# Kernel optimization log

Measured on AMD Instinct MI355X. Metric: run time of the kernel, lower is better.

Reference implementation:

```python
import jax, jax.numpy as jnp
import numpy as np

B, T, N, H, DK = 4, 16, 256, 8, 64

def setup_inputs() -> dict:
    key = jax.random.key(0)
    k1, k2, k3 = jax.random.split(key, 3)
    queries = jax.random.normal(k1, (B, T, N, H, DK), dtype=jnp.float32)
    keys = jax.random.normal(k2, (B, T, N, H, DK), dtype=jnp.float32)
    values = jax.random.normal(k3, (B, T, N, H, DK), dtype=jnp.float32)
    attention_mask = jnp.zeros((B, T, 1, N, N), dtype=bool)  # unused: mask_flag=False
    return {"queries": queries, "keys": keys, "values": values, "attention_mask": attention_mask}

def reference(queries, keys, values, attention_mask):
    # queries: B T N H d_k; keys/values: B T S H d_k/d_v
    d_k = queries.shape[-1]
    scale = 1.0 / jnp.sqrt(jnp.asarray(d_k, queries.dtype))
    # scores: B T H N S
    scores = jnp.einsum('btnhe,btshe->bthns', queries, keys)
    # mask_flag=False -> no masking; dropout is identity in eval mode
    A = jax.nn.softmax(scale * scores, axis=-1)
    V = jnp.einsum('bthns,btshd->btnhd', A, values)
    return V
```

## Files before the change

### kernel.cpp

```cpp
#include <hip/hip_runtime.h>


typedef short short8 __attribute__((ext_vector_type(8)));
typedef float floatx16 __attribute__((ext_vector_type(16)));

__device__ __forceinline__ unsigned cvt_pk(float lo, float hi) {
  unsigned r;
  asm("v_cvt_pk_bf16_f32 %0, %1, %2" : "=v"(r) : "v"(lo), "v"(hi));
  return r;
}

constexpr int KSTR  = 72;
constexpr int VSTRW = 132;

__global__ __launch_bounds__(512, 2) void attn_kernel(
    const float* __restrict__ Q, const float* __restrict__ K,
    const float* __restrict__ V, float* __restrict__ O) {
  __shared__ __align__(16) short    Klds[256 * KSTR];
  __shared__ __align__(16) unsigned Vt32[64 * VSTRW];

  const int inst = blockIdx.x;
  const int h8   = inst & 7;
  const int bt   = inst >> 3;
  const int base = bt * (256 * 512) + h8 * 64;
  const int tid  = threadIdx.x;

  const int wave = tid >> 6;
  const int lane = tid & 63;
  const int r31  = lane & 31;
  const int h    = lane >> 5;
  const int c4   = tid & 15;
  const int sQ   = tid >> 4;

  {
    const float* Kb = K + base;
    #pragma unroll
    for (int i = 0; i < 8; ++i) {
      int idx = i * 512 + tid;
      int s = idx >> 4, cc = idx & 15;
      float4 v = *reinterpret_cast<const float4*>(Kb + s * 512 + cc * 4);
      uint2 w;
      w.x = cvt_pk(v.x, v.y);
      w.y = cvt_pk(v.z, v.w);
      *reinterpret_cast<uint2*>(&Klds[s * KSTR + cc * 4]) = w;
    }
  }
  {
    const float* Vb = V + base;
    #pragma unroll
    for (int i = 0; i < 4; ++i) {
      int idx = i * 512 + tid;
      int sp = idx >> 4, cc = idx & 15;
      int s = sp * 2;
      int spw = sp ^ ((cc & 7) << 2);
      float4 v0 = *reinterpret_cast<const float4*>(Vb + s * 512 + cc * 4);
      float4 v1 = *reinterpret_cast<const float4*>(Vb + (s + 1) * 512 + cc * 4);
      #pragma unroll
      for (int k = 0; k < 4; ++k)
        Vt32[(cc * 4 + k) * VSTRW + spw] = cvt_pk((&v0.x)[k], (&v1.x)[k]);
    }
  }

  const float SCQ = 0.125f * 1.4426950408889634f;
  const int nq = wave * 32 + r31;
  short8 qf[4];
  #pragma unroll
  for (int kc = 0; kc < 4; ++kc) {
    const float* qp = Q + base + nq * 512 + 16 * kc + 8 * h;
    float4 a = *reinterpret_cast<const float4*>(qp);
    float4 b = *reinterpret_cast<const float4*>(qp + 4);
    union { unsigned u[4]; short8 s; } t;
    t.u[0] = cvt_pk(a.x * SCQ, a.y * SCQ);
    t.u[1] = cvt_pk(a.z * SCQ, a.w * SCQ);
    t.u[2] = cvt_pk(b.x * SCQ, b.y * SCQ);
    t.u[3] = cvt_pk(b.z * SCQ, b.w * SCQ);
    qf[kc] = t.s;
  }
  __syncthreads();

  const int swzr = ((r31 >> 2) & 7) << 2;

  floatx16 ao0 = {}, ao1 = {};
  float ps[4] = {0.f, 0.f, 0.f, 0.f};

  #pragma unroll
  for (int it = 0; it < 8; ++it) {
    floatx16 sc = {};
    #pragma unroll
    for (int kc = 0; kc < 4; ++kc) {
      short8 kf = *reinterpret_cast<const short8*>(
          &Klds[(32 * it + r31) * KSTR + 16 * kc + 8 * h]);
      sc = __builtin_amdgcn_mfma_f32_32x32x16_bf16(kf, qf[kc], sc, 0, 0, 0);
    }

    unsigned pk[8];
    #pragma unroll
    for (int q = 0; q < 4; ++q) {
      float e0 = exp2f(sc[4 * q + 0]);
      float e1 = exp2f(sc[4 * q + 1]);
      float e2 = exp2f(sc[4 * q + 2]);
      float e3 = exp2f(sc[4 * q + 3]);
      ps[q] += (e0 + e1) + (e2 + e3);
      pk[2 * q]     = cvt_pk(e0, e1);
      pk[2 * q + 1] = cvt_pk(e2, e3);
    }

    union { unsigned u[4]; short8 s; } pa0, pa1;
    {
      unsigned x, y;
      x = pk[0]; y = pk[2];
      asm("v_permlane32_swap_b32 %0, %1" : "+v"(x), "+v"(y));
      pa0.u[0] = x; pa0.u[2] = y;
      x = pk[1]; y = pk[3];
      asm("v_permlane32_swap_b32 %0, %1" : "+v"(x), "+v"(y));
      pa0.u[1] = x; pa0.u[3] = y;
      x = pk[4]; y = pk[6];
      asm("v_permlane32_swap_b32 %0, %1" : "+v"(x), "+v"(y));
      pa1.u[0] = x; pa1.u[2] = y;
      x = pk[5]; y = pk[7];
      asm("v_permlane32_swap_b32 %0, %1" : "+v"(x), "+v"(y));
      pa1.u[1] = x; pa1.u[3] = y;
    }

    {
      const unsigned* vrow0 = &Vt32[(r31) * VSTRW];
      const unsigned* vrow1 = &Vt32[(32 + r31) * VSTRW];
      short8 vf00 = *reinterpret_cast<const short8*>(
          vrow0 + ((16 * it + 4 * h) ^ swzr));
      short8 vf01 = *reinterpret_cast<const short8*>(
          vrow0 + ((16 * it + 8 + 4 * h) ^ swzr));
      short8 vf10 = *reinterpret_cast<const short8*>(
          vrow1 + ((16 * it + 4 * h) ^ swzr));
      short8 vf11 = *reinterpret_cast<const short8*>(
          vrow1 + ((16 * it + 8 + 4 * h) ^ swzr));
      ao0 = __builtin_amdgcn_mfma_f32_32x32x16_bf16(pa0.s, vf00, ao0, 0, 0, 0);
      ao0 = __builtin_amdgcn_mfma_f32_32x32x16_bf16(pa1.s, vf01, ao0, 0, 0, 0);
      ao1 = __builtin_amdgcn_mfma_f32_32x32x16_bf16(pa0.s, vf10, ao1, 0, 0, 0);
      ao1 = __builtin_amdgcn_mfma_f32_32x32x16_bf16(pa1.s, vf11, ao1, 0, 0, 0);
    }
  }

  float pstot = (ps[0] + ps[1]) + (ps[2] + ps[3]);
  pstot += __shfl_xor(pstot, 32);
  const float rcp = __builtin_amdgcn_rcpf(pstot);

  float rcpv[16];
  #pragma unroll
  for (int reg = 0; reg < 16; ++reg)
    rcpv[reg] = __shfl(rcp, (reg & 3) + 8 * (reg >> 2) + 4 * h);

  #pragma unroll
  for (int reg = 0; reg < 16; ++reg) {
    int n = wave * 32 + (reg & 3) + 8 * (reg >> 2) + 4 * h;
    O[base + n * 512 + r31]      = ao0[reg] * rcpv[reg];
    O[base + n * 512 + 32 + r31] = ao1[reg] * rcpv[reg];
  }
}

extern "C" void kernel_launch(void* const* d_in, const int* in_sizes, int n_in,
                              void* d_out, int out_size, void* d_ws, size_t ws_size,
                              hipStream_t stream) {
  const float* Q = (const float*)d_in[0];
  const float* K = (const float*)d_in[1];
  const float* V = (const float*)d_in[2];
  float* O = (float*)d_out;
  attn_kernel<<<dim3(512), dim3(512), 0, stream>>>(Q, K, V, O);
}
```

Before: 33.80 us.

## Process two heads per block with double-buffered LDS and 16x16 MFMA tiles

Each 1024-thread block now handles two (bt,head) instances. K/V for the second instance are staged into a second LDS buffer while the first is being computed, which is meant to hide global load latency. The attention math switches from 32x32x16 to 16x16x32 MFMAs with 16 queries per wave, using permlane16/32 swaps to rebuild the P operand. The grid is halved to 256 blocks, which cuts the number of active workgroups on a 256-CU part and raises register and LDS pressure per block.

```diff
diff --git a/kernel.cpp b/kernel.cpp
--- a/kernel.cpp
+++ b/kernel.cpp
@@ -2,7 +2,7 @@
 
 
 typedef short short8 __attribute__((ext_vector_type(8)));
-typedef float floatx16 __attribute__((ext_vector_type(16)));
+typedef float floatx4 __attribute__((ext_vector_type(4)));
 
 __device__ __forceinline__ unsigned cvt_pk(float lo, float hi) {
   unsigned r;
@@ -13,148 +13,151 @@
 constexpr int KSTR  = 72;
 constexpr int VSTRW = 132;
 
-__global__ __launch_bounds__(512, 2) void attn_kernel(
+__device__ __forceinline__ void stage_kv(const float* __restrict__ Kb,
+                                         const float* __restrict__ Vb,
+                                         short* Kl, unsigned* Vt, int tid) {
+  #pragma unroll
+  for (int i = 0; i < 4; ++i) {
+    int idx = i * 1024 + tid;
+    int s = idx >> 4, cc = idx & 15;
+    float4 v = *reinterpret_cast<const float4*>(Kb + s * 512 + cc * 4);
+    uint2 w;
+    w.x = cvt_pk(v.x, v.y);
+    w.y = cvt_pk(v.z, v.w);
+    *reinterpret_cast<uint2*>(&Kl[s * KSTR + cc * 4]) = w;
+  }
+  #pragma unroll
+  for (int i = 0; i < 2; ++i) {
+    int idx = i * 1024 + tid;
+    int sp = idx >> 4, cc = idx & 15;
+    int s = sp * 2;
+    int spw = sp ^ ((cc & 7) << 2);
+    float4 v0 = *reinterpret_cast<const float4*>(Vb + s * 512 + cc * 4);
+    float4 v1 = *reinterpret_cast<const float4*>(Vb + (s + 1) * 512 + cc * 4);
+    #pragma unroll
+    for (int k = 0; k < 4; ++k)
+      Vt[(cc * 4 + k) * VSTRW + spw] = cvt_pk((&v0.x)[k], (&v1.x)[k]);
+  }
+}
+
+__global__ __launch_bounds__(1024, 4) void attn_kernel(
     const float* __restrict__ Q, const float* __restrict__ K,
     const float* __restrict__ V, float* __restrict__ O) {
-  __shared__ __align__(16) short    Klds[256 * KSTR];
-  __shared__ __align__(16) unsigned Vt32[64 * VSTRW];
+  __shared__ __align__(16) short    Klds[2][256 * KSTR];
+  __shared__ __align__(16) unsigned Vt32[2][64 * VSTRW];
 
-  const int inst = blockIdx.x;
-  const int h8   = inst & 7;
-  const int bt   = inst >> 3;
-  const int base = bt * (256 * 512) + h8 * 64;
   const int tid  = threadIdx.x;
-
   const int wave = tid >> 6;
   const int lane = tid & 63;
-  const int r31  = lane & 31;
-  const int h    = lane >> 5;
-  const int c4   = tid & 15;
-  const int sQ   = tid >> 4;
+  const int c    = lane & 15;
+  const int g    = lane >> 4;
 
-  {
-    const float* Kb = K + base;
-    #pragma unroll
-    for (int i = 0; i < 8; ++i) {
-      int idx = i * 512 + tid;
-      int s = idx >> 4, cc = idx & 15;
-      float4 v = *reinterpret_cast<const float4*>(Kb + s * 512 + cc * 4);
-      uint2 w;
-      w.x = cvt_pk(v.x, v.y);
-      w.y = cvt_pk(v.z, v.w);
-      *reinterpret_cast<uint2*>(&Klds[s * KSTR + cc * 4]) = w;
-    }
-  }
-  {
-    const float* Vb = V + base;
-    #pragma unroll
-    for (int i = 0; i < 4; ++i) {
-      int idx = i * 512 + tid;
-      int sp = idx >> 4, cc = idx & 15;
-      int s = sp * 2;
-      int spw = sp ^ ((cc & 7) << 2);
-      float4 v0 = *reinterpret_cast<const float4*>(Vb + s * 512 + cc * 4);
-      float4 v1 = *reinterpret_cast<const float4*>(Vb + (s + 1) * 512 + cc * 4);
-      #pragma unroll
-      for (int k = 0; k < 4; ++k)
-        Vt32[(cc * 4 + k) * VSTRW + spw] = cvt_pk((&v0.x)[k], (&v1.x)[k]);
-    }
+  const int i0    = blockIdx.x * 2;
+  const int i1    = i0 + 1;
+  const int base0 = (i0 >> 3) * (256 * 512) + (i0 & 7) * 64;
+  const int base1 = (i1 >> 3) * (256 * 512) + (i1 & 7) * 64;
+
+  const float SCQ = 0.125f * 1.4426950408889634f;
+
+#define LOADQ(qf, gbase)                                                     \
+  {                                                                          \
+    _Pragma("unroll")                                                        \
+    for (int ks2 = 0; ks2 < 2; ++ks2) {                                      \
+      const float* qp = Q + (gbase) + (wave * 16 + c) * 512 + ks2 * 32 + g * 8; \
+      float4 a  = *reinterpret_cast<const float4*>(qp);                      \
+      float4 bb = *reinterpret_cast<const float4*>(qp + 4);                  \
+      union { unsigned u[4]; short8 s; } t;                                  \
+      t.u[0] = cvt_pk(a.x * SCQ, a.y * SCQ);                                 \
+      t.u[1] = cvt_pk(a.z * SCQ, a.w * SCQ);                                 \
+      t.u[2] = cvt_pk(bb.x * SCQ, bb.y * SCQ);                               \
+      t.u[3] = cvt_pk(bb.z * SCQ, bb.w * SCQ);                               \
+      qf[ks2] = t.s;                                                         \
+    }                                                                        \
   }
 
-  const float SCQ = 0.125f * 1.4426950408889634f;
-  const int nq = wave * 32 + r31;
-  short8 qf[4];
-  #pragma unroll
-  for (int kc = 0; kc < 4; ++kc) {
-    const float* qp = Q + base + nq * 512 + 16 * kc + 8 * h;
-    float4 a = *reinterpret_cast<const float4*>(qp);
-    float4 b = *reinterpret_cast<const float4*>(qp + 4);
-    union { unsigned u[4]; short8 s; } t;
-    t.u[0] = cvt_pk(a.x * SCQ, a.y * SCQ);
-    t.u[1] = cvt_pk(a.z * SCQ, a.w * SCQ);
-    t.u[2] = cvt_pk(b.x * SCQ, b.y * SCQ);
-    t.u[3] = cvt_pk(b.z * SCQ, b.w * SCQ);
-    qf[kc] = t.s;
+#define COMPUTE(b, qf, ao, ps)                                               \
+  _Pragma("unroll")                                                          \
+  for (int ks = 0; ks < 8; ++ks) {                                           \
+    unsigned pk2[2][2];                                                      \
+    _Pragma("unroll")                                                        \
+    for (int tt = 0; tt < 2; ++tt) {                                         \
+      const int t = 2 * ks + tt;                                             \
+      short8 kf0 = *reinterpret_cast<const short8*>(                         \
+          &Klds[b][(t * 16 + c) * KSTR + g * 8]);                            \
+      short8 kf1 = *reinterpret_cast<const short8*>(                         \
+          &Klds[b][(t * 16 + c) * KSTR + 32 + g * 8]);                       \
+      floatx4 acc = {0.f, 0.f, 0.f, 0.f};                                    \
+      acc = __builtin_amdgcn_mfma_f32_16x16x32_bf16(kf0, qf[0], acc, 0, 0, 0); \
+      acc = __builtin_amdgcn_mfma_f32_16x16x32_bf16(kf1, qf[1], acc, 0, 0, 0); \
+      float e0 = exp2f(acc[0]);                                              \
+      float e1 = exp2f(acc[1]);                                              \
+      float e2 = exp2f(acc[2]);                                              \
+      float e3 = exp2f(acc[3]);                                              \
+      ps[0] += e0; ps[1] += e1; ps[2] += e2; ps[3] += e3;                    \
+      pk2[tt][0] = cvt_pk(e0, e1);                                           \
+      pk2[tt][1] = cvt_pk(e2, e3);                                           \
+    }                                                                        \
+    union { unsigned u[4]; short8 s; } pa;                                   \
+    _Pragma("unroll")                                                        \
+    for (int m = 0; m < 2; ++m) {                                            \
+      unsigned x = pk2[0][m], y = pk2[1][m];                                 \
+      asm("v_permlane32_swap_b32 %0, %1" : "+v"(x), "+v"(y));                \
+      asm("v_permlane16_swap_b32 %0, %1" : "+v"(x), "+v"(y));                \
+      pa.u[m]     = x;                                                       \
+      pa.u[2 + m] = y;                                                       \
+    }                                                                        \
+    _Pragma("unroll")                                                        \
+    for (int dt = 0; dt < 4; ++dt) {                                         \
+      short8 vf = *reinterpret_cast<const short8*>(                          \
+          reinterpret_cast<const short*>(                                    \
+              &Vt32[b][(dt * 16 + c) * VSTRW +                               \
+                       ((ks * 16 + 4 * g) ^ (16 * (dt & 1) + (c & 12)))]));  \
+      ao[dt] = __builtin_amdgcn_mfma_f32_16x16x32_bf16(pa.s, vf, ao[dt], 0, 0, 0); \
+    }                                                                        \
   }
+
+#define EPILOGUE(ao, ps, gbase)                                              \
+  {                                                                          \
+    float s4 = (ps[0] + ps[1]) + (ps[2] + ps[3]);                            \
+    s4 += __shfl_xor(s4, 16);                                                \
+    s4 += __shfl_xor(s4, 32);                                                \
+    const float rcp = __builtin_amdgcn_rcpf(s4);                             \
+    float rcpv[4];                                                           \
+    _Pragma("unroll")                                                        \
+    for (int r = 0; r < 4; ++r) rcpv[r] = __shfl(rcp, 4 * g + r);            \
+    _Pragma("unroll")                                                        \
+    for (int dt = 0; dt < 4; ++dt)                                           \
+      _Pragma("unroll")                                                      \
+      for (int r = 0; r < 4; ++r)                                            \
+        O[(gbase) + (wave * 16 + 4 * g + r) * 512 + dt * 16 + c] =           \
+            ao[dt][r] * rcpv[r];                                             \
+  }
+
+  short8 qf0[2], qf1[2];
+  LOADQ(qf0, base0);
+  stage_kv(K + base0, V + base0, Klds[0], Vt32[0], tid);
   __syncthreads();
 
-  const int swzr = ((r31 >> 2) & 7) << 2;
+  LOADQ(qf1, base1);
+  stage_kv(K + base1, V + base1, Klds[1], Vt32[1], tid);
 
-  floatx16 ao0 = {}, ao1 = {};
-  float ps[4] = {0.f, 0.f, 0.f, 0.f};
+  floatx4 ao0[4] = {{0.f,0.f,0.f,0.f},{0.f,0.f,0.f,0.f},
+                    {0.f,0.f,0.f,0.f},{0.f,0.f,0.f,0.f}};
+  float ps0[4] = {0.f, 0.f, 0.f, 0.f};
+  COMPUTE(0, qf0, ao0, ps0);
+  __syncthreads();
 
-  #pragma unroll
-  for (int it = 0; it < 8; ++it) {
-    floatx16 sc = {};
-    #pragma unroll
-    for (int kc = 0; kc < 4; ++kc) {
-      short8 kf = *reinterpret_cast<const short8*>(
-          &Klds[(32 * it + r31) * KSTR + 16 * kc + 8 * h]);
-      sc = __builtin_amdgcn_mfma_f32_32x32x16_bf16(kf, qf[kc], sc, 0, 0, 0);
-    }
+  EPILOGUE(ao0, ps0, base0);
 
-    unsigned pk[8];
-    #pragma unroll
-    for (int q = 0; q < 4; ++q) {
-      float e0 = exp2f(sc[4 * q + 0]);
-      float e1 = exp2f(sc[4 * q + 1]);
-      float e2 = exp2f(sc[4 * q + 2]);
-      float e3 = exp2f(sc[4 * q + 3]);
-      ps[q] += (e0 + e1) + (e2 + e3);
-      pk[2 * q]     = cvt_pk(e0, e1);
-      pk[2 * q + 1] = cvt_pk(e2, e3);
-    }
+  floatx4 ao1[4] = {{0.f,0.f,0.f,0.f},{0.f,0.f,0.f,0.f},
+                    {0.f,0.f,0.f,0.f},{0.f,0.f,0.f,0.f}};
+  float ps1[4] = {0.f, 0.f, 0.f, 0.f};
+  COMPUTE(1, qf1, ao1, ps1);
+  EPILOGUE(ao1, ps1, base1);
 
-    union { unsigned u[4]; short8 s; } pa0, pa1;
-    {
-      unsigned x, y;
-      x = pk[0]; y = pk[2];
-      asm("v_permlane32_swap_b32 %0, %1" : "+v"(x), "+v"(y));
-      pa0.u[0] = x; pa0.u[2] = y;
-      x = pk[1]; y = pk[3];
-      asm("v_permlane32_swap_b32 %0, %1" : "+v"(x), "+v"(y));
-      pa0.u[1] = x; pa0.u[3] = y;
-      x = pk[4]; y = pk[6];
-      asm("v_permlane32_swap_b32 %0, %1" : "+v"(x), "+v"(y));
-      pa1.u[0] = x; pa1.u[2] = y;
-      x = pk[5]; y = pk[7];
-      asm("v_permlane32_swap_b32 %0, %1" : "+v"(x), "+v"(y));
-      pa1.u[1] = x; pa1.u[3] = y;
-    }
-
-    {
-      const unsigned* vrow0 = &Vt32[(r31) * VSTRW];
-      const unsigned* vrow1 = &Vt32[(32 + r31) * VSTRW];
-      short8 vf00 = *reinterpret_cast<const short8*>(
-          vrow0 + ((16 * it + 4 * h) ^ swzr));
-      short8 vf01 = *reinterpret_cast<const short8*>(
-          vrow0 + ((16 * it + 8 + 4 * h) ^ swzr));
-      short8 vf10 = *reinterpret_cast<const short8*>(
-          vrow1 + ((16 * it + 4 * h) ^ swzr));
-      short8 vf11 = *reinterpret_cast<const short8*>(
-          vrow1 + ((16 * it + 8 + 4 * h) ^ swzr));
-      ao0 = __builtin_amdgcn_mfma_f32_32x32x16_bf16(pa0.s, vf00, ao0, 0, 0, 0);
-      ao0 = __builtin_amdgcn_mfma_f32_32x32x16_bf16(pa1.s, vf01, ao0, 0, 0, 0);
-      ao1 = __builtin_amdgcn_mfma_f32_32x32x16_bf16(pa0.s, vf10, ao1, 0, 0, 0);
-      ao1 = __builtin_amdgcn_mfma_f32_32x32x16_bf16(pa1.s, vf11, ao1, 0, 0, 0);
-    }
-  }
-
-  float pstot = (ps[0] + ps[1]) + (ps[2] + ps[3]);
-  pstot += __shfl_xor(pstot, 32);
-  const float rcp = __builtin_amdgcn_rcpf(pstot);
-
-  float rcpv[16];
-  #pragma unroll
-  for (int reg = 0; reg < 16; ++reg)
-    rcpv[reg] = __shfl(rcp, (reg & 3) + 8 * (reg >> 2) + 4 * h);
-
-  #pragma unroll
-  for (int reg = 0; reg < 16; ++reg) {
-    int n = wave * 32 + (reg & 3) + 8 * (reg >> 2) + 4 * h;
-    O[base + n * 512 + r31]      = ao0[reg] * rcpv[reg];
-    O[base + n * 512 + 32 + r31] = ao1[reg] * rcpv[reg];
-  }
+#undef LOADQ
+#undef COMPUTE
+#undef EPILOGUE
 }
 
 extern "C" void kernel_launch(void* const* d_in, const int* in_sizes, int n_in,
@@ -164,5 +167,5 @@
   const float* K = (const float*)d_in[1];
   const float* V = (const float*)d_in[2];
   float* O = (float*)d_out;
-  attn_kernel<<<dim3(512), dim3(512), 0, stream>>>(Q, K, V, O);
+  attn_kernel<<<dim3(256), dim3(1024), 0, stream>>>(Q, K, V, O);
 }
```

After: 32.33 us. 1.05x faster.
